# Optimization experiments

Measured on AMD Instinct MI355X. Metric: run time of the kernel, lower is better.

The kernel has to match this reference:

```python
import jax, jax.numpy as jnp
import numpy as np

OUT_H = 7
OUT_W = 7
C = 256
SPATIAL_SCALE = 0.0625
SAMPLING_RATIO = 2
GAMMA = 0.1
SIGMA = 0.5
FDIM = OUT_H * OUT_W * C  # 12544
DFC = 1024
B, H, W = 4, 100, 152
N_ROIS = 512
IMG_H, IMG_W = H / SPATIAL_SCALE, W / SPATIAL_SCALE


def _bilinear(feat, b, y, x):
    # feat: [B,H,W,C]; b int32 and y,x float coords, mutually broadcastable.
    Hf, Wf = feat.shape[1], feat.shape[2]
    valid = (y > -1.0) & (y < Hf) & (x > -1.0) & (x < Wf)
    yc = jnp.clip(y, 0.0, Hf - 1.0)
    xc = jnp.clip(x, 0.0, Wf - 1.0)
    y0 = jnp.clip(jnp.floor(yc).astype(jnp.int32), 0, Hf - 2)
    x0 = jnp.clip(jnp.floor(xc).astype(jnp.int32), 0, Wf - 2)
    ly = yc - y0.astype(yc.dtype)
    lx = xc - x0.astype(xc.dtype)
    hy, hx = 1.0 - ly, 1.0 - lx
    val = ((hy * hx)[..., None] * feat[b, y0, x0]
           + (hy * lx)[..., None] * feat[b, y0, x0 + 1]
           + (ly * hx)[..., None] * feat[b, y0 + 1, x0]
           + (ly * lx)[..., None] * feat[b, y0 + 1, x0 + 1])
    return jnp.where(valid[..., None], val, jnp.zeros((), val.dtype))


def deform_roi_pool(inp, rois, offset):
    # mmcv DeformRoIPool semantics; rois get no gradient (torch returns None).
    rois = jax.lax.stop_gradient(rois)
    feat = jnp.transpose(inp, (0, 2, 3, 1))  # [B,H,W,C]
    n = rois.shape[0]
    b = rois[:, 0].astype(jnp.int32)[:, None, None, None, None]
    x1 = rois[:, 1] * SPATIAL_SCALE - 0.5
    y1 = rois[:, 2] * SPATIAL_SCALE - 0.5
    x2 = rois[:, 3] * SPATIAL_SCALE - 0.5
    y2 = rois[:, 4] * SPATIAL_SCALE - 0.5
    rw, rh = x2 - x1, y2 - y1
    bw, bh = rw / OUT_W, rh / OUT_H
    start_w = jnp.broadcast_to(x1[:, None, None], (n, OUT_H, OUT_W))
    start_h = jnp.broadcast_to(y1[:, None, None], (n, OUT_H, OUT_W))
    if offset is not None:
        start_w = start_w + GAMMA * rw[:, None, None] * offset[:, 0]
        start_h = start_h + GAMMA * rh[:, None, None] * offset[:, 1]
    g = (jnp.arange(SAMPLING_RATIO, dtype=inp.dtype) + 0.5) / SAMPLING_RATIO
    ph = jnp.arange(OUT_H, dtype=inp.dtype)
    pw = jnp.arange(OUT_W, dtype=inp.dtype)
    # per-bin sample coords: ys,xs -> [n,oh,ow,g]
    ys = start_h[..., None] + (ph[None, :, None, None] + g) * bh[:, None, None, None]
    xs = start_w[..., None] + (pw[None, None, :, None] + g) * bw[:, None, None, None]
    yy = ys[..., :, None]  # [n,oh,ow,g,1]
    xx = xs[..., None, :]  # [n,oh,ow,1,g]
    val = _bilinear(feat, b, yy, xx)  # [n,oh,ow,g,g,C]
    out = val.mean(axis=(3, 4))  # count = g*g samples per bin
    return jnp.transpose(out, (0, 3, 1, 2))  # [n,C,oh,ow]


def _make_rois(key, n):
    k1, k2, k3, k4, k5 = jax.random.split(key, 5)
    bi = jax.random.randint(k1, (n,), 0, B).astype(jnp.float32)
    cx = jax.random.uniform(k2, (n,)) * IMG_W
    cy = jax.random.uniform(k3, (n,)) * IMG_H
    w = 32.0 + jax.random.uniform(k4, (n,)) * 300.0
    h = 32.0 + jax.random.uniform(k5, (n,)) * 300.0
    x1 = jnp.clip(cx - 0.5 * w, 0.0, IMG_W - 1.0)
    x2 = jnp.clip(cx + 0.5 * w, 0.0, IMG_W - 1.0)
    y1 = jnp.clip(cy - 0.5 * h, 0.0, IMG_H - 1.0)
    y2 = jnp.clip(cy + 0.5 * h, 0.0, IMG_H - 1.0)
    return jnp.stack([bi, x1, y1, x2, y2], axis=1)


def setup_inputs() -> dict:
    key = jax.random.key(0)
    ks = jax.random.split(key, 12)
    inp = jax.random.normal(ks[0], (B, C, H, W), dtype=jnp.float32)
    rois = _make_rois(ks[1], N_ROIS)
    s = 0.02
    return {
        'input': inp,
        'rois': rois,
        'rescale_w': s * jax.random.normal(ks[2], (OUT_H * OUT_W * 2, FDIM), jnp.float32),
        'rescale_b': s * jax.random.normal(ks[3], (OUT_H * OUT_W * 2,), jnp.float32),
        'off_w1': s * jax.random.normal(ks[4], (DFC, FDIM), jnp.float32),
        'off_b1': s * jax.random.normal(ks[5], (DFC,), jnp.float32),
        'off_w2': s * jax.random.normal(ks[6], (DFC, DFC), jnp.float32),
        'off_b2': s * jax.random.normal(ks[7], (DFC,), jnp.float32),
        'off_w3': s * jax.random.normal(ks[8], (OUT_H * OUT_W * 2, DFC), jnp.float32),
        'off_b3': s * jax.random.normal(ks[9], (OUT_H * OUT_W * 2,), jnp.float32),
    }


def reference(input, rois, rescale_w, rescale_b, off_w1, off_b1, off_w2, off_b2, off_w3, off_b3):
    x_cls = deform_roi_pool(input, rois, None)  # [N,C,7,7]
    n = rois.shape[0]
    flat = x_cls.reshape(n, -1)  # torch .view(N,-1) on NCHW layout
    rescale = 1.0 + SIGMA * jax.nn.sigmoid(flat @ rescale_w.T + rescale_b)
    # rescale_roi uses only columns 0..3 of the rescale head output
    cx = (rois[:, 1] + rois[:, 3]) * 0.5 + rescale[:, 0]
    cy = (rois[:, 2] + rois[:, 4]) * 0.5 + rescale[:, 1]
    nw = (rois[:, 3] - rois[:, 1]) * rescale[:, 2]
    nh = (rois[:, 4] - rois[:, 2]) * rescale[:, 3]
    new_rois = jnp.stack([rois[:, 0], cx - 0.5 * nw, cy - 0.5 * nh,
                          cx + 0.5 * nw, cy + 0.5 * nh], axis=-1)
    h1 = jax.nn.relu(flat @ off_w1.T + off_b1)
    h2 = jax.nn.relu(h1 @ off_w2.T + off_b2)
    off = (h2 @ off_w3.T + off_b3).reshape(n, 2, OUT_H, OUT_W)
    x_reg = deform_roi_pool(input, new_rois, off)
    return x_cls, x_reg
```

## Files before the change

### kernel.cpp

```cpp
#include <hip/hip_runtime.h>
#include <math.h>

#define NCH 256
#define HH 100
#define WW 152
#define BB 4
#define NROIS 512
#define FDIM 12544
#define DFC 1024
#define HW 15200

typedef unsigned short u16;
typedef float f32x2 __attribute__((ext_vector_type(2)));
typedef float f32x4 __attribute__((ext_vector_type(4)));
typedef short s16x8 __attribute__((ext_vector_type(8)));
typedef __bf16 bf16x8 __attribute__((ext_vector_type(8)));

__device__ __forceinline__ u16 f2bf(float f) {
  union { float f; unsigned u; } c; c.f = f;
  unsigned u = c.u;
  return (u16)((u + 0x7FFFu + ((u >> 16) & 1u)) >> 16);
}
__device__ __forceinline__ float bf2f(u16 h) {
  union { unsigned u; float f; } c; c.u = ((unsigned)h) << 16;
  return c.f;
}

template<int WITH_OFF>
__global__ __launch_bounds__(256) void pool_nchw(
    const float* __restrict__ feat, const float* __restrict__ rois,
    const float* __restrict__ offp, float* __restrict__ out) {
  const int n    = blockIdx.x;
  const int tid  = threadIdx.x;
  const int wave = tid >> 6;
  const int lane = tid & 63;
  float r[5];
  const float* rp = rois + n * 5;
  #pragma unroll
  for (int i = 0; i < 5; ++i) r[i] = rp[i];
  int b = (int)r[0];
  b = min(max(b, 0), BB - 1);
  const float x1 = r[1] * 0.0625f - 0.5f;
  const float y1 = r[2] * 0.0625f - 0.5f;
  const float x2 = r[3] * 0.0625f - 0.5f;
  const float y2 = r[4] * 0.0625f - 0.5f;
  const float rw = x2 - x1, rh = y2 - y1;
  const float bw = rw * (1.0f / 7.0f), bh = rh * (1.0f / 7.0f);
  const int bin = lane;
  const bool active = (bin < 49);
  const int ph = bin / 7;
  const int pw = bin - ph * 7;
  float sw = x1, sh = y1;
  if (WITH_OFF && active) {
    sw += 0.1f * rw * offp[n * 98 + bin];
    sh += 0.1f * rh * offp[n * 98 + 49 + bin];
  }
  int idx[4];
  float wt[4][4];
  bool val[4];
  #pragma unroll
  for (int s = 0; s < 4; ++s) {
    const int i = s >> 1, j = s & 1;
    const float y = sh + ((float)ph + 0.25f + 0.5f * (float)i) * bh;
    const float x = sw + ((float)pw + 0.25f + 0.5f * (float)j) * bw;
    val[s] = active && (y > -1.0f) && (y < (float)HH) && (x > -1.0f) && (x < (float)WW);
    float yc = fminf(fmaxf(y, 0.f), (float)(HH - 1));
    float xc = fminf(fmaxf(x, 0.f), (float)(WW - 1));
    int y0 = min(max((int)floorf(yc), 0), HH - 2);
    int x0 = min(max((int)floorf(xc), 0), WW - 2);
    const float ly = yc - (float)y0, lx = xc - (float)x0;
    const float hy = 1.f - ly, hx = 1.f - lx;
    idx[s] = y0 * WW + x0;
    wt[s][0] = hy * hx; wt[s][1] = hy * lx;
    wt[s][2] = ly * hx; wt[s][3] = ly * lx;
  }
  const float* fb = feat + (size_t)b * NCH * HW;
  float* op = out + (size_t)n * FDIM;
  for (int c = wave; c < NCH; c += 4) {
    const float* plane = fb + (size_t)c * HW;
    float acc = 0.f;
    #pragma unroll
    for (int s = 0; s < 4; ++s) {
      if (val[s]) {
        const float* p = plane + idx[s];
        acc += wt[s][0] * p[0] + wt[s][1] * p[1]
             + wt[s][2] * p[WW] + wt[s][3] * p[WW + 1];
      }
    }
    if (active) op[c * 49 + bin] = acc * 0.25f;
  }
}

__global__ __launch_bounds__(256) void nchw_to_nhwc(
    const float* __restrict__ in, float* __restrict__ outp) {
  __shared__ float tile[64][65];
  const int b  = blockIdx.z;
  const int c0 = blockIdx.y * 64;
  const int p0 = blockIdx.x * 64;
  const int tx = threadIdx.x & 63;
  const int ty = threadIdx.x >> 6;
  const float* ib = in + ((size_t)b * NCH + c0) * HW + p0;
  #pragma unroll
  for (int i = 0; i < 16; ++i) {
    const int r = ty + i * 4;
    tile[r][tx] = (p0 + tx < HW) ? ib[(size_t)r * HW + tx] : 0.f;
  }
  __syncthreads();
  float* ob = outp + ((size_t)b * HW + p0) * NCH + c0;
  #pragma unroll
  for (int i = 0; i < 16; ++i) {
    const int pr = ty + i * 4;
    if (p0 + pr < HW) ob[(size_t)pr * NCH + tx] = tile[tx][pr];
  }
}

template<int WITH_OFF, int SPLIT>
__global__ __launch_bounds__(256) void pool_nhwc_cg(
    const float* __restrict__ feat, const float* __restrict__ rois,
    const float* __restrict__ offp, float* __restrict__ out,
    u16* __restrict__ ahi, u16* __restrict__ alo) {
  __shared__ float obuf[64 * 49];
  const int n  = blockIdx.x;
  const int cg = blockIdx.y;
  const int w    = threadIdx.x >> 6;
  const int lane = threadIdx.x & 63;
  const int c = cg * 64 + lane;
  float r[5];
  const float* rp = rois + n * 5;
  #pragma unroll
  for (int i = 0; i < 5; ++i) r[i] = rp[i];
  int b = (int)r[0];
  b = min(max(b, 0), BB - 1);
  const float x1 = r[1] * 0.0625f - 0.5f;
  const float y1 = r[2] * 0.0625f - 0.5f;
  const float x2 = r[3] * 0.0625f - 0.5f;
  const float y2 = r[4] * 0.0625f - 0.5f;
  const float rw = x2 - x1, rh = y2 - y1;
  const float bw = rw * (1.0f / 7.0f), bh = rh * (1.0f / 7.0f);
  const float* fb = feat + (size_t)b * HW * NCH + c;
  for (int bin = w; bin < 49; bin += 4) {
    const int ph = bin / 7;
    const int pw = bin - ph * 7;
    float sw = x1, sh = y1;
    if (WITH_OFF) {
      sw += 0.1f * rw * offp[n * 98 + bin];
      sh += 0.1f * rh * offp[n * 98 + 49 + bin];
    }
    float acc = 0.f;
    #pragma unroll
    for (int s = 0; s < 4; ++s) {
      const int i = s >> 1, j = s & 1;
      const float y = sh + ((float)ph + 0.25f + 0.5f * (float)i) * bh;
      const float x = sw + ((float)pw + 0.25f + 0.5f * (float)j) * bw;
      const bool val = (y > -1.0f) && (y < (float)HH) && (x > -1.0f) && (x < (float)WW);
      float yc = fminf(fmaxf(y, 0.f), (float)(HH - 1));
      float xc = fminf(fmaxf(x, 0.f), (float)(WW - 1));
      int y0 = min(max((int)floorf(yc), 0), HH - 2);
      int x0 = min(max((int)floorf(xc), 0), WW - 2);
      const float ly = yc - (float)y0, lx = xc - (float)x0;
      const float hy = 1.f - ly, hx = 1.f - lx;
      if (val) {
        const float* p = fb + ((size_t)y0 * WW + x0) * NCH;
        acc += (hy * hx) * p[0] + (hy * lx) * p[NCH]
             + (ly * hx) * p[WW * NCH] + (ly * lx) * p[WW * NCH + NCH];
      }
    }
    obuf[lane * 49 + bin] = acc * 0.25f;
  }
  __syncthreads();
  const size_t base = (size_t)n * FDIM + (size_t)cg * (64 * 49);
  float* op = out + base;
  for (int i = threadIdx.x; i < 64 * 49; i += 256) {
    const float v = obuf[i];
    op[i] = v;
    if (SPLIT) {
      const u16 h = f2bf(v);
      ahi[base + i] = h;
      alo[base + i] = f2bf(v - bf2f(h));
    }
  }
}

__global__ __launch_bounds__(256) void rescale_rois_kernel(
    const float* __restrict__ flat, const float* __restrict__ w,
    const float* __restrict__ bsc, const float* __restrict__ rois,
    float* __restrict__ new_rois) {
  __shared__ float red[4];
  const int n = blockIdx.x;
  const int j = threadIdx.x >> 6;
  const int lane = threadIdx.x & 63;
  const float* a = flat + (size_t)n * FDIM;
  const float* wj = w + (size_t)j * FDIM;
  float acc = 0.f;
  for (int k = lane * 8; k + 8 <= FDIM; k += 64 * 8) {
    f32x4 a0 = *(const f32x4*)(a + k);
    f32x4 a1 = *(const f32x4*)(a + k + 4);
    f32x4 w0 = *(const f32x4*)(wj + k);
    f32x4 w1 = *(const f32x4*)(wj + k + 4);
    float s = 0.f;
    #pragma unroll
    for (int e = 0; e < 4; ++e) s += a0[e] * w0[e];
    #pragma unroll
    for (int e = 0; e < 4; ++e) s += a1[e] * w1[e];
    acc += s;
  }
  #pragma unroll
  for (int d = 32; d > 0; d >>= 1)
    acc += __shfl_down(acc, d, 64);
  if (lane == 0) red[j] = acc;
  __syncthreads();
  if (threadIdx.x == 0) {
    float rr[5];
    const float* rp = rois + n * 5;
    #pragma unroll
    for (int i = 0; i < 5; ++i) rr[i] = rp[i];
    float sc[4];
    #pragma unroll
    for (int jj = 0; jj < 4; ++jj) {
      const float z = red[jj] + bsc[jj];
      sc[jj] = 1.0f + 0.5f / (1.0f + expf(-z));
    }
    const float cx = (rr[1] + rr[3]) * 0.5f + sc[0];
    const float cy = (rr[2] + rr[4]) * 0.5f + sc[1];
    const float nw = (rr[3] - rr[1]) * sc[2];
    const float nh = (rr[4] - rr[2]) * sc[3];
    float* o = new_rois + n * 5;
    o[0] = rr[0];
    o[1] = cx - 0.5f * nw;
    o[2] = cy - 0.5f * nh;
    o[3] = cx + 0.5f * nw;
    o[4] = cy + 0.5f * nh;
  }
}

__global__ __launch_bounds__(512, 4) void gemm_mfma_sk(
    const float* __restrict__ A, const float* __restrict__ B,
    float* __restrict__ part, int M, int N, int Ns, int K, int kchunk) {
  __shared__ __align__(16) u16 Ah[64 * 32];
  __shared__ __align__(16) u16 Al[64 * 32];
  __shared__ __align__(16) u16 Bh[128 * 32];
  __shared__ __align__(16) u16 Bl[128 * 32];
  const int tid  = threadIdx.x;
  const int wave = tid >> 6;
  const int lane = tid & 63;
  const int q  = lane >> 4;
  const int rr = lane & 15;
  const int wr = wave >> 2;
  const int wc = wave & 3;
  const int m0 = blockIdx.y * 64;
  const int n0 = blockIdx.x * 128;
  const int s  = blockIdx.z;
  const int kb = s * kchunk, ke = kb + kchunk;

  const int srow  = tid >> 2;
  const int sslot = tid & 3;
  const int swz   = sslot ^ ((srow >> 1) & 3);
  const bool astage = tid < 256;
  u16* const a_sth = &Ah[srow * 32 + swz * 8];
  u16* const a_stl = &Al[srow * 32 + swz * 8];
  u16* const b_sth = &Bh[srow * 32 + swz * 8];
  u16* const b_stl = &Bl[srow * 32 + swz * 8];
  const float* Ap = A + (size_t)(m0 + (astage ? srow : 0)) * K + sslot * 8;
  const int  brow = n0 + srow;
  const bool bok  = brow < N;
  const float* Bp = B + (size_t)(bok ? brow : 0) * K + sslot * 8;

  const int rsw = q ^ ((rr >> 1) & 3);
  const u16* const a_rdh = &Ah[(wr * 32 + rr) * 32 + rsw * 8];
  const u16* const a_rdl = &Al[(wr * 32 + rr) * 32 + rsw * 8];
  const u16* const b_rdh = &Bh[(wc * 32 + rr) * 32 + rsw * 8];
  const u16* const b_rdl = &Bl[(wc * 32 + rr) * 32 + rsw * 8];

  f32x4 acc[2][2];
  #pragma unroll
  for (int mt = 0; mt < 2; ++mt)
    #pragma unroll
    for (int nt = 0; nt < 2; ++nt) acc[mt][nt] = (f32x4){0.f, 0.f, 0.f, 0.f};

  for (int k0 = kb; k0 < ke; k0 += 32) {
    f32x4 a0 = (f32x4){0.f, 0.f, 0.f, 0.f}, a1 = a0, b0 = a0, b1 = a0;
    if (astage) { a0 = *(const f32x4*)(Ap + k0); a1 = *(const f32x4*)(Ap + k0 + 4); }
    if (bok)    { b0 = *(const f32x4*)(Bp + k0); b1 = *(const f32x4*)(Bp + k0 + 4); }
    bf16x8 avh, avl, bvh, bvl;
    #pragma unroll
    for (int e = 0; e < 4; ++e) {
      const __bf16 h0 = (__bf16)a0[e], h1 = (__bf16)a1[e];
      avh[e] = h0; avh[e + 4] = h1;
      avl[e]     = (__bf16)(a0[e] - (float)h0);
      avl[e + 4] = (__bf16)(a1[e] - (float)h1);
      const __bf16 g0 = (__bf16)b0[e], g1 = (__bf16)b1[e];
      bvh[e] = g0; bvh[e + 4] = g1;
      bvl[e]     = (__bf16)(b0[e] - (float)g0);
      bvl[e + 4] = (__bf16)(b1[e] - (float)g1);
    }
    __syncthreads();
    if (astage) { *(bf16x8*)a_sth = avh; *(bf16x8*)a_stl = avl; }
    *(bf16x8*)b_sth = bvh;
    *(bf16x8*)b_stl = bvl;
    __syncthreads();
    bf16x8 ah[2], al[2], bh[2], bl[2];
    #pragma unroll
    for (int mt = 0; mt < 2; ++mt) {
      ah[mt] = *(const bf16x8*)(a_rdh + mt * 16 * 32);
      al[mt] = *(const bf16x8*)(a_rdl + mt * 16 * 32);
    }
    #pragma unroll
    for (int nt = 0; nt < 2; ++nt) {
      bh[nt] = *(const bf16x8*)(b_rdh + nt * 16 * 32);
      bl[nt] = *(const bf16x8*)(b_rdl + nt * 16 * 32);
    }
    #pragma unroll
    for (int mt = 0; mt < 2; ++mt)
      #pragma unroll
      for (int nt = 0; nt < 2; ++nt) {
        acc[mt][nt] = __builtin_amdgcn_mfma_f32_16x16x32_bf16(ah[mt], bh[nt], acc[mt][nt], 0, 0, 0);
        acc[mt][nt] = __builtin_amdgcn_mfma_f32_16x16x32_bf16(al[mt], bh[nt], acc[mt][nt], 0, 0, 0);
        acc[mt][nt] = __builtin_amdgcn_mfma_f32_16x16x32_bf16(ah[mt], bl[nt], acc[mt][nt], 0, 0, 0);
      }
  }

  float* pb = part + (size_t)s * M * Ns;
  #pragma unroll
  for (int mt = 0; mt < 2; ++mt)
    #pragma unroll
    for (int nt = 0; nt < 2; ++nt) {
      const int col = n0 + wc * 32 + nt * 16 + rr;
      #pragma unroll
      for (int i = 0; i < 4; ++i) {
        const int row = m0 + wr * 32 + mt * 16 + q * 4 + i;
        pb[(size_t)row * Ns + col] = acc[mt][nt][i];
      }
    }
}

__global__ __launch_bounds__(512) void gemm_mfma_ps_sk(
    const u16* __restrict__ Ahi, const u16* __restrict__ Alo,
    const float* __restrict__ B,
    float* __restrict__ part, int M, int N, int Ns, int K, int kchunk) {
  __shared__ __align__(16) u16 AhB[2][64 * 32];
  __shared__ __align__(16) u16 AlB[2][64 * 32];
  __shared__ __align__(16) u16 BhB[2][128 * 32];
  __shared__ __align__(16) u16 BlB[2][128 * 32];
  const int tid  = threadIdx.x;
  const int wave = tid >> 6;
  const int lane = tid & 63;
  const int q  = lane >> 4;
  const int rr = lane & 15;
  const int wr = wave >> 2;
  const int wc = wave & 3;
  const int m0 = blockIdx.y * 64;
  const int n0 = blockIdx.x * 128;
  const int s  = blockIdx.z;
  const int kb = s * kchunk, ke = kb + kchunk;

  const int srow  = tid >> 2;
  const int sslot = tid & 3;
  const int swz   = sslot ^ ((srow >> 1) & 3);
  const bool astage = tid < 256;
  const int ast = srow * 32 + swz * 8;
  const u16* Aph = Ahi + (size_t)(m0 + (astage ? srow : 0)) * K + sslot * 8;
  const u16* Apl = Alo + (size_t)(m0 + (astage ? srow : 0)) * K + sslot * 8;
  const int  brow = n0 + srow;
  const bool bok  = brow < N;
  const float* Bp = B + (size_t)(bok ? brow : 0) * K + sslot * 8;

  const int rsw = q ^ ((rr >> 1) & 3);
  const int ard = (wr * 32 + rr) * 32 + rsw * 8;
  const int brd = (wc * 32 + rr) * 32 + rsw * 8;

  f32x4 acc[2][2];
  #pragma unroll
  for (int mt = 0; mt < 2; ++mt)
    #pragma unroll
    for (int nt = 0; nt < 2; ++nt) acc[mt][nt] = (f32x4){0.f, 0.f, 0.f, 0.f};

  {
    s16x8 avh, avl;
    f32x4 b0 = (f32x4){0.f, 0.f, 0.f, 0.f}, b1 = b0;
    if (astage) { avh = *(const s16x8*)(Aph + kb); avl = *(const s16x8*)(Apl + kb); }
    if (bok)    { b0 = *(const f32x4*)(Bp + kb); b1 = *(const f32x4*)(Bp + kb + 4); }
    bf16x8 bvh, bvl;
    #pragma unroll
    for (int e = 0; e < 4; ++e) {
      const __bf16 g0 = (__bf16)b0[e], g1 = (__bf16)b1[e];
      bvh[e] = g0; bvh[e + 4] = g1;
      bvl[e]     = (__bf16)(b0[e] - (float)g0);
      bvl[e + 4] = (__bf16)(b1[e] - (float)g1);
    }
    if (astage) { *(s16x8*)&AhB[0][ast] = avh; *(s16x8*)&AlB[0][ast] = avl; }
    *(bf16x8*)&BhB[0][ast] = bvh;
    *(bf16x8*)&BlB[0][ast] = bvl;
  }
  __syncthreads();

  int cur = 0;
  for (int k0 = kb; k0 < ke; k0 += 32) {
    const bool nx = (k0 + 32 < ke);
    s16x8 navh, navl;
    f32x4 nb0 = (f32x4){0.f, 0.f, 0.f, 0.f}, nb1 = nb0;
    if (nx) {
      if (astage) {
        navh = *(const s16x8*)(Aph + k0 + 32);
        navl = *(const s16x8*)(Apl + k0 + 32);
      }
      if (bok) {
        nb0 = *(const f32x4*)(Bp + k0 + 32);
        nb1 = *(const f32x4*)(Bp + k0 + 36);
      }
    }
    bf16x8 ah[2], al[2], bh2[2], bl2[2];
    #pragma unroll
    for (int mt = 0; mt < 2; ++mt) {
      ah[mt] = *(const bf16x8*)&AhB[cur][ard + mt * 16 * 32];
      al[mt] = *(const bf16x8*)&AlB[cur][ard + mt * 16 * 32];
    }
    #pragma unroll
    for (int nt = 0; nt < 2; ++nt) {
      bh2[nt] = *(const bf16x8*)&BhB[cur][brd + nt * 16 * 32];
      bl2[nt] = *(const bf16x8*)&BlB[cur][brd + nt * 16 * 32];
    }
    #pragma unroll
    for (int mt = 0; mt < 2; ++mt)
      #pragma unroll
      for (int nt = 0; nt < 2; ++nt) {
        acc[mt][nt] = __builtin_amdgcn_mfma_f32_16x16x32_bf16(ah[mt], bh2[nt], acc[mt][nt], 0, 0, 0);
        acc[mt][nt] = __builtin_amdgcn_mfma_f32_16x16x32_bf16(al[mt], bh2[nt], acc[mt][nt], 0, 0, 0);
        acc[mt][nt] = __builtin_amdgcn_mfma_f32_16x16x32_bf16(ah[mt], bl2[nt], acc[mt][nt], 0, 0, 0);
      }
    if (nx) {
      bf16x8 nbvh, nbvl;
      #pragma unroll
      for (int e = 0; e < 4; ++e) {
        const __bf16 g0 = (__bf16)nb0[e], g1 = (__bf16)nb1[e];
        nbvh[e] = g0; nbvh[e + 4] = g1;
        nbvl[e]     = (__bf16)(nb0[e] - (float)g0);
        nbvl[e + 4] = (__bf16)(nb1[e] - (float)g1);
      }
      if (astage) { *(s16x8*)&AhB[cur ^ 1][ast] = navh; *(s16x8*)&AlB[cur ^ 1][ast] = navl; }
      *(bf16x8*)&BhB[cur ^ 1][ast] = nbvh;
      *(bf16x8*)&BlB[cur ^ 1][ast] = nbvl;
    }
    __syncthreads();
    cur ^= 1;
  }

  float* pb = part + (size_t)s * M * Ns;
  #pragma unroll
  for (int mt = 0; mt < 2; ++mt)
    #pragma unroll
    for (int nt = 0; nt < 2; ++nt) {
      const int col = n0 + wc * 32 + nt * 16 + rr;
      #pragma unroll
      for (int i = 0; i < 4; ++i) {
        const int row = m0 + wr * 32 + mt * 16 + q * 4 + i;
        pb[(size_t)row * Ns + col] = acc[mt][nt][i];
      }
    }
}

template<int RELU>
__global__ __launch_bounds__(256) void reduce_sk(
    const float* __restrict__ part, const float* __restrict__ bias,
    float* __restrict__ out, int M, int N, int Ns, int S) {
  const int idx = blockIdx.x * 256 + threadIdx.x;
  if (idx >= M * Ns) return;
  const int m = idx / Ns, n = idx - m * Ns;
  if (n >= N) return;
  float v = bias[n];
  for (int s = 0; s < S; ++s) v += part[(size_t)s * M * Ns + idx];
  if (RELU) v = fmaxf(v, 0.f);
  out[(size_t)m * N + n] = v;
}

__global__ __launch_bounds__(256) void reduce_sk_split(
    const float* __restrict__ part, const float* __restrict__ bias,
    u16* __restrict__ oh, u16* __restrict__ ol, int M, int N, int S) {
  const int idx = blockIdx.x * 256 + threadIdx.x;
  if (idx >= M * N) return;
  const int n = idx % N;
  float v = bias[n];
  for (int s = 0; s < S; ++s) v += part[(size_t)s * M * N + idx];
  v = fmaxf(v, 0.f);
  const u16 h = f2bf(v);
  oh[idx] = h;
  ol[idx] = f2bf(v - bf2f(h));
}

extern "C" void kernel_launch(void* const* d_in, const int* in_sizes, int n_in,
                              void* d_out, int out_size, void* d_ws, size_t ws_size,
                              hipStream_t stream) {
  const float* input  = (const float*)d_in[0];
  const float* rois   = (const float*)d_in[1];
  const float* resc_w = (const float*)d_in[2];
  const float* resc_b = (const float*)d_in[3];
  const float* w1     = (const float*)d_in[4];
  const float* b1     = (const float*)d_in[5];
  const float* w2     = (const float*)d_in[6];
  const float* b2     = (const float*)d_in[7];
  const float* w3     = (const float*)d_in[8];
  const float* b3     = (const float*)d_in[9];
  float* out = (float*)d_out;

  char* ws = (char*)d_ws;
  const size_t feat_t_bytes = (size_t)BB * HW * NCH * sizeof(float);

  float* part    = (float*)ws;
  u16*   h1h     = (u16*)(ws + (16u << 20));
  u16*   h1l     = (u16*)(ws + (17u << 20));
  u16*   h2h     = (u16*)(ws + (18u << 20));
  u16*   h2l     = (u16*)(ws + (19u << 20));
  float* offbuf2 = (float*)(ws + (20u << 20));
  float* nrois2  = (float*)(ws + (20u << 20) + 512 * 1024);
  u16*   Ahi     = (u16*)(ws + (21u << 20));
  u16*   Alo     = (u16*)(ws + (34u << 20));
  float* feat_t2 = (float*)(ws + (47u << 20));
  const bool big2 = ws_size >= ((size_t)(47u << 20) + feat_t_bytes);

  float* h1     = (float*)(ws + (16u << 20));
  float* h2     = (float*)(ws + (18u << 20));
  float* offbuf = (float*)(ws + (22u << 20));
  float* nrois  = (float*)(ws + (22u << 20) + 256 * 1024);
  float* feat_t = (float*)(ws + ((size_t)24 << 20));
  const bool big = ws_size >= (((size_t)24 << 20) + feat_t_bytes);

  float* x_cls = out;
  float* x_reg = out + (size_t)NROIS * FDIM;

  if (big2) {
    nchw_to_nhwc<<<dim3(238, 4, 4), 256, 0, stream>>>(input, feat_t2);
    pool_nhwc_cg<0, 1><<<dim3(NROIS, 4), 256, 0, stream>>>(feat_t2, rois, nullptr, x_cls, Ahi, Alo);
    rescale_rois_kernel<<<NROIS, 256, 0, stream>>>(x_cls, resc_w, resc_b, rois, nrois2);

    gemm_mfma_ps_sk<<<dim3(8, 8, 8), 512, 0, stream>>>(Ahi, Alo, w1, part, NROIS, DFC, DFC, FDIM, FDIM / 8);
    reduce_sk_split<<<(NROIS * DFC + 255) / 256, 256, 0, stream>>>(part, b1, h1h, h1l, NROIS, DFC, 8);
    gemm_mfma_ps_sk<<<dim3(8, 8, 8), 512, 0, stream>>>(h1h, h1l, w2, part, NROIS, DFC, DFC, DFC, DFC / 8);
    reduce_sk_split<<<(NROIS * DFC + 255) / 256, 256, 0, stream>>>(part, b2, h2h, h2l, NROIS, DFC, 8);
    gemm_mfma_ps_sk<<<dim3(1, 8, 8), 512, 0, stream>>>(h2h, h2l, w3, part, NROIS, 98, 128, DFC, DFC / 8);
    reduce_sk<0><<<(NROIS * 128 + 255) / 256, 256, 0, stream>>>(part, b3, offbuf2, NROIS, 98, 128, 8);

    pool_nhwc_cg<1, 0><<<dim3(NROIS, 4), 256, 0, stream>>>(feat_t2, nrois2, offbuf2, x_reg, nullptr, nullptr);
  } else if (big) {
    nchw_to_nhwc<<<dim3(238, 4, 4), 256, 0, stream>>>(input, feat_t);
    pool_nhwc_cg<0, 0><<<dim3(NROIS, 4), 256, 0, stream>>>(feat_t, rois, nullptr, x_cls, nullptr, nullptr);
    rescale_rois_kernel<<<NROIS, 256, 0, stream>>>(x_cls, resc_w, resc_b, rois, nrois);

    gemm_mfma_sk<<<dim3(8, 8, 8), 512, 0, stream>>>(x_cls, w1, part, NROIS, DFC, DFC, FDIM, FDIM / 8);
    reduce_sk<1><<<(NROIS * DFC + 255) / 256, 256, 0, stream>>>(part, b1, h1, NROIS, DFC, DFC, 8);
    gemm_mfma_sk<<<dim3(8, 8, 8), 512, 0, stream>>>(h1, w2, part, NROIS, DFC, DFC, DFC, DFC / 8);
    reduce_sk<1><<<(NROIS * DFC + 255) / 256, 256, 0, stream>>>(part, b2, h2, NROIS, DFC, DFC, 8);
    gemm_mfma_sk<<<dim3(1, 8, 8), 512, 0, stream>>>(h2, w3, part, NROIS, 98, 128, DFC, DFC / 8);
    reduce_sk<0><<<(NROIS * 128 + 255) / 256, 256, 0, stream>>>(part, b3, offbuf, NROIS, 98, 128, 8);

    pool_nhwc_cg<1, 0><<<dim3(NROIS, 4), 256, 0, stream>>>(feat_t, nrois, offbuf, x_reg, nullptr, nullptr);
  } else {
    pool_nchw<0><<<NROIS, 256, 0, stream>>>(input, rois, nullptr, x_cls);
    rescale_rois_kernel<<<NROIS, 256, 0, stream>>>(x_cls, resc_w, resc_b, rois, nrois);
    gemm_mfma_sk<<<dim3(8, 8, 8), 512, 0, stream>>>(x_cls, w1, part, NROIS, DFC, DFC, FDIM, FDIM / 8);
    reduce_sk<1><<<(NROIS * DFC + 255) / 256, 256, 0, stream>>>(part, b1, h1, NROIS, DFC, DFC, 8);
    gemm_mfma_sk<<<dim3(8, 8, 8), 512, 0, stream>>>(h1, w2, part, NROIS, DFC, DFC, DFC, DFC / 8);
    reduce_sk<1><<<(NROIS * DFC + 255) / 256, 256, 0, stream>>>(part, b2, h2, NROIS, DFC, DFC, 8);
    gemm_mfma_sk<<<dim3(1, 8, 8), 512, 0, stream>>>(h2, w3, part, NROIS, 98, 128, DFC, DFC / 8);
    reduce_sk<0><<<(NROIS * 128 + 255) / 256, 256, 0, stream>>>(part, b3, offbuf, NROIS, 98, 128, 8);
    pool_nchw<1><<<NROIS, 256, 0, stream>>>(input, nrois, offbuf, x_reg);
  }
}
```

Baseline: 359.0 us.

## Single-buffer split-precision GEMM, raise occupancy, and deepen split-K for first layer

Replaces the register-prefetched double-buffered LDS pipeline in the split-bf16 GEMM with a single-buffered loop that loads, stores and syncs twice per K step. It adds a launch-bounds occupancy hint of 4 blocks per CU. When the workspace is large enough, the first FC layer's split-K factor goes from 8 to 14 to launch more blocks, using a larger partial-sum buffer. The aim is more resident waves to hide latency, at the cost of losing explicit prefetch overlap and an extra barrier per iteration.

```diff
diff --git a/kernel.cpp b/kernel.cpp
--- a/kernel.cpp
+++ b/kernel.cpp
@@ -11,7 +11,6 @@
 #define HW 15200
 
 typedef unsigned short u16;
-typedef float f32x2 __attribute__((ext_vector_type(2)));
 typedef float f32x4 __attribute__((ext_vector_type(4)));
 typedef short s16x8 __attribute__((ext_vector_type(8)));
 typedef __bf16 bf16x8 __attribute__((ext_vector_type(8)));
@@ -333,14 +332,14 @@
     }
 }
 
-__global__ __launch_bounds__(512) void gemm_mfma_ps_sk(
+__global__ __launch_bounds__(512, 4) void gemm_ps(
     const u16* __restrict__ Ahi, const u16* __restrict__ Alo,
     const float* __restrict__ B,
     float* __restrict__ part, int M, int N, int Ns, int K, int kchunk) {
-  __shared__ __align__(16) u16 AhB[2][64 * 32];
-  __shared__ __align__(16) u16 AlB[2][64 * 32];
-  __shared__ __align__(16) u16 BhB[2][128 * 32];
-  __shared__ __align__(16) u16 BlB[2][128 * 32];
+  __shared__ __align__(16) u16 Ah[64 * 32];
+  __shared__ __align__(16) u16 Al[64 * 32];
+  __shared__ __align__(16) u16 Bh[128 * 32];
+  __shared__ __align__(16) u16 Bl[128 * 32];
   const int tid  = threadIdx.x;
   const int wave = tid >> 6;
   const int lane = tid & 63;
@@ -357,7 +356,10 @@
   const int sslot = tid & 3;
   const int swz   = sslot ^ ((srow >> 1) & 3);
   const bool astage = tid < 256;
-  const int ast = srow * 32 + swz * 8;
+  u16* const a_sth = &Ah[srow * 32 + swz * 8];
+  u16* const a_stl = &Al[srow * 32 + swz * 8];
+  u16* const b_sth = &Bh[srow * 32 + swz * 8];
+  u16* const b_stl = &Bl[srow * 32 + swz * 8];
   const u16* Aph = Ahi + (size_t)(m0 + (astage ? srow : 0)) * K + sslot * 8;
   const u16* Apl = Alo + (size_t)(m0 + (astage ? srow : 0)) * K + sslot * 8;
   const int  brow = n0 + srow;
@@ -365,8 +367,10 @@
   const float* Bp = B + (size_t)(bok ? brow : 0) * K + sslot * 8;
 
   const int rsw = q ^ ((rr >> 1) & 3);
-  const int ard = (wr * 32 + rr) * 32 + rsw * 8;
-  const int brd = (wc * 32 + rr) * 32 + rsw * 8;
+  const u16* const a_rdh = &Ah[(wr * 32 + rr) * 32 + rsw * 8];
+  const u16* const a_rdl = &Al[(wr * 32 + rr) * 32 + rsw * 8];
+  const u16* const b_rdh = &Bh[(wc * 32 + rr) * 32 + rsw * 8];
+  const u16* const b_rdl = &Bl[(wc * 32 + rr) * 32 + rsw * 8];
 
   f32x4 acc[2][2];
   #pragma unroll
@@ -374,11 +378,11 @@
     #pragma unroll
     for (int nt = 0; nt < 2; ++nt) acc[mt][nt] = (f32x4){0.f, 0.f, 0.f, 0.f};
 
-  {
+  for (int k0 = kb; k0 < ke; k0 += 32) {
     s16x8 avh, avl;
     f32x4 b0 = (f32x4){0.f, 0.f, 0.f, 0.f}, b1 = b0;
-    if (astage) { avh = *(const s16x8*)(Aph + kb); avl = *(const s16x8*)(Apl + kb); }
-    if (bok)    { b0 = *(const f32x4*)(Bp + kb); b1 = *(const f32x4*)(Bp + kb + 4); }
+    if (astage) { avh = *(const s16x8*)(Aph + k0); avl = *(const s16x8*)(Apl + k0); }
+    if (bok)    { b0 = *(const f32x4*)(Bp + k0); b1 = *(const f32x4*)(Bp + k0 + 4); }
     bf16x8 bvh, bvl;
     #pragma unroll
     for (int e = 0; e < 4; ++e) {
@@ -387,61 +391,30 @@
       bvl[e]     = (__bf16)(b0[e] - (float)g0);
       bvl[e + 4] = (__bf16)(b1[e] - (float)g1);
     }
-    if (astage) { *(s16x8*)&AhB[0][ast] = avh; *(s16x8*)&AlB[0][ast] = avl; }
-    *(bf16x8*)&BhB[0][ast] = bvh;
-    *(bf16x8*)&BlB[0][ast] = bvl;
-  }
-  __syncthreads();
-
-  int cur = 0;
-  for (int k0 = kb; k0 < ke; k0 += 32) {
-    const bool nx = (k0 + 32 < ke);
-    s16x8 navh, navl;
-    f32x4 nb0 = (f32x4){0.f, 0.f, 0.f, 0.f}, nb1 = nb0;
-    if (nx) {
-      if (astage) {
-        navh = *(const s16x8*)(Aph + k0 + 32);
-        navl = *(const s16x8*)(Apl + k0 + 32);
-      }
-      if (bok) {
-        nb0 = *(const f32x4*)(Bp + k0 + 32);
-        nb1 = *(const f32x4*)(Bp + k0 + 36);
-      }
-    }
-    bf16x8 ah[2], al[2], bh2[2], bl2[2];
+    __syncthreads();
+    if (astage) { *(s16x8*)a_sth = avh; *(s16x8*)a_stl = avl; }
+    *(bf16x8*)b_sth = bvh;
+    *(bf16x8*)b_stl = bvl;
+    __syncthreads();
+    bf16x8 ah[2], al[2], bh[2], bl[2];
     #pragma unroll
     for (int mt = 0; mt < 2; ++mt) {
-      ah[mt] = *(const bf16x8*)&AhB[cur][ard + mt * 16 * 32];
-      al[mt] = *(const bf16x8*)&AlB[cur][ard + mt * 16 * 32];
+      ah[mt] = *(const bf16x8*)(a_rdh + mt * 16 * 32);
+      al[mt] = *(const bf16x8*)(a_rdl + mt * 16 * 32);
     }
     #pragma unroll
     for (int nt = 0; nt < 2; ++nt) {
-      bh2[nt] = *(const bf16x8*)&BhB[cur][brd + nt * 16 * 32];
-      bl2[nt] = *(const bf16x8*)&BlB[cur][brd + nt * 16 * 32];
+      bh[nt] = *(const bf16x8*)(b_rdh + nt * 16 * 32);
+      bl[nt] = *(const bf16x8*)(b_rdl + nt * 16 * 32);
     }
     #pragma unroll
     for (int mt = 0; mt < 2; ++mt)
       #pragma unroll
       for (int nt = 0; nt < 2; ++nt) {
-        acc[mt][nt] = __builtin_amdgcn_mfma_f32_16x16x32_bf16(ah[mt], bh2[nt], acc[mt][nt], 0, 0, 0);
-        acc[mt][nt] = __builtin_amdgcn_mfma_f32_16x16x32_bf16(al[mt], bh2[nt], acc[mt][nt], 0, 0, 0);
-        acc[mt][nt] = __builtin_amdgcn_mfma_f32_16x16x32_bf16(ah[mt], bl2[nt], acc[mt][nt], 0, 0, 0);
+        acc[mt][nt] = __builtin_amdgcn_mfma_f32_16x16x32_bf16(ah[mt], bh[nt], acc[mt][nt], 0, 0, 0);
+        acc[mt][nt] = __builtin_amdgcn_mfma_f32_16x16x32_bf16(al[mt], bh[nt], acc[mt][nt], 0, 0, 0);
+        acc[mt][nt] = __builtin_amdgcn_mfma_f32_16x16x32_bf16(ah[mt], bl[nt], acc[mt][nt], 0, 0, 0);
       }
-    if (nx) {
-      bf16x8 nbvh, nbvl;
-      #pragma unroll
-      for (int e = 0; e < 4; ++e) {
-        const __bf16 g0 = (__bf16)nb0[e], g1 = (__bf16)nb1[e];
-        nbvh[e] = g0; nbvh[e + 4] = g1;
-        nbvl[e]     = (__bf16)(nb0[e] - (float)g0);
-        nbvl[e + 4] = (__bf16)(nb1[e] - (float)g1);
-      }
-      if (astage) { *(s16x8*)&AhB[cur ^ 1][ast] = navh; *(s16x8*)&AlB[cur ^ 1][ast] = navl; }
-      *(bf16x8*)&BhB[cur ^ 1][ast] = nbvh;
-      *(bf16x8*)&BlB[cur ^ 1][ast] = nbvl;
-    }
-    __syncthreads();
-    cur ^= 1;
   }
 
   float* pb = part + (size_t)s * M * Ns;
@@ -504,42 +477,64 @@
   char* ws = (char*)d_ws;
   const size_t feat_t_bytes = (size_t)BB * HW * NCH * sizeof(float);
 
-  float* part    = (float*)ws;
-  u16*   h1h     = (u16*)(ws + (16u << 20));
-  u16*   h1l     = (u16*)(ws + (17u << 20));
-  u16*   h2h     = (u16*)(ws + (18u << 20));
-  u16*   h2l     = (u16*)(ws + (19u << 20));
-  float* offbuf2 = (float*)(ws + (20u << 20));
-  float* nrois2  = (float*)(ws + (20u << 20) + 512 * 1024);
-  u16*   Ahi     = (u16*)(ws + (21u << 20));
-  u16*   Alo     = (u16*)(ws + (34u << 20));
-  float* feat_t2 = (float*)(ws + (47u << 20));
-  const bool big2 = ws_size >= ((size_t)(47u << 20) + feat_t_bytes);
-
-  float* h1     = (float*)(ws + (16u << 20));
-  float* h2     = (float*)(ws + (18u << 20));
-  float* offbuf = (float*)(ws + (22u << 20));
-  float* nrois  = (float*)(ws + (22u << 20) + 256 * 1024);
-  float* feat_t = (float*)(ws + ((size_t)24 << 20));
-  const bool big = ws_size >= (((size_t)24 << 20) + feat_t_bytes);
-
   float* x_cls = out;
   float* x_reg = out + (size_t)NROIS * FDIM;
 
-  if (big2) {
+  const bool big3 = ws_size >= (((size_t)59 << 20) + feat_t_bytes);
+  const bool big2 = ws_size >= (((size_t)47 << 20) + feat_t_bytes);
+  const bool big = ws_size >= (((size_t)24 << 20) + feat_t_bytes);
+
+  if (big3 || big2) {
+    float* part;
+    u16 *h1h, *h1l, *h2h, *h2l, *Ahi, *Alo;
+    float *offbuf2, *nrois2, *feat_t2;
+    int S1;
+    if (big3) {
+      part    = (float*)ws;
+      h1h     = (u16*)(ws + ((size_t)28 << 20));
+      h1l     = (u16*)(ws + ((size_t)29 << 20));
+      h2h     = (u16*)(ws + ((size_t)30 << 20));
+      h2l     = (u16*)(ws + ((size_t)31 << 20));
+      offbuf2 = (float*)(ws + ((size_t)32 << 20));
+      nrois2  = (float*)(ws + ((size_t)32 << 20) + 512 * 1024);
+      Ahi     = (u16*)(ws + ((size_t)33 << 20));
+      Alo     = (u16*)(ws + ((size_t)46 << 20));
+      feat_t2 = (float*)(ws + ((size_t)59 << 20));
+      S1 = 14;
+    } else {
+      part    = (float*)ws;
+      h1h     = (u16*)(ws + ((size_t)16 << 20));
+      h1l     = (u16*)(ws + ((size_t)17 << 20));
+      h2h     = (u16*)(ws + ((size_t)18 << 20));
+      h2l     = (u16*)(ws + ((size_t)19 << 20));
+      offbuf2 = (float*)(ws + ((size_t)20 << 20));
+      nrois2  = (float*)(ws + ((size_t)20 << 20) + 512 * 1024);
+      Ahi     = (u16*)(ws + ((size_t)21 << 20));
+      Alo     = (u16*)(ws + ((size_t)34 << 20));
+      feat_t2 = (float*)(ws + ((size_t)47 << 20));
+      S1 = 8;
+    }
+
     nchw_to_nhwc<<<dim3(238, 4, 4), 256, 0, stream>>>(input, feat_t2);
     pool_nhwc_cg<0, 1><<<dim3(NROIS, 4), 256, 0, stream>>>(feat_t2, rois, nullptr, x_cls, Ahi, Alo);
     rescale_rois_kernel<<<NROIS, 256, 0, stream>>>(x_cls, resc_w, resc_b, rois, nrois2);
 
-    gemm_mfma_ps_sk<<<dim3(8, 8, 8), 512, 0, stream>>>(Ahi, Alo, w1, part, NROIS, DFC, DFC, FDIM, FDIM / 8);
-    reduce_sk_split<<<(NROIS * DFC + 255) / 256, 256, 0, stream>>>(part, b1, h1h, h1l, NROIS, DFC, 8);
-    gemm_mfma_ps_sk<<<dim3(8, 8, 8), 512, 0, stream>>>(h1h, h1l, w2, part, NROIS, DFC, DFC, DFC, DFC / 8);
+    gemm_ps<<<dim3(8, 8, S1), 512, 0, stream>>>(Ahi, Alo, w1, part, NROIS, DFC, DFC, FDIM, FDIM / S1);
+    reduce_sk_split<<<(NROIS * DFC + 255) / 256, 256, 0, stream>>>(part, b1, h1h, h1l, NROIS, DFC, S1);
+    gemm_ps<<<dim3(8, 8, 8), 512, 0, stream>>>(h1h, h1l, w2, part, NROIS, DFC, DFC, DFC, DFC / 8);
     reduce_sk_split<<<(NROIS * DFC + 255) / 256, 256, 0, stream>>>(part, b2, h2h, h2l, NROIS, DFC, 8);
-    gemm_mfma_ps_sk<<<dim3(1, 8, 8), 512, 0, stream>>>(h2h, h2l, w3, part, NROIS, 98, 128, DFC, DFC / 8);
+    gemm_ps<<<dim3(1, 8, 8), 512, 0, stream>>>(h2h, h2l, w3, part, NROIS, 98, 128, DFC, DFC / 8);
     reduce_sk<0><<<(NROIS * 128 + 255) / 256, 256, 0, stream>>>(part, b3, offbuf2, NROIS, 98, 128, 8);
 
     pool_nhwc_cg<1, 0><<<dim3(NROIS, 4), 256, 0, stream>>>(feat_t2, nrois2, offbuf2, x_reg, nullptr, nullptr);
   } else if (big) {
+    float* part   = (float*)ws;
+    float* h1     = (float*)(ws + ((size_t)16 << 20));
+    float* h2     = (float*)(ws + ((size_t)18 << 20));
+    float* offbuf = (float*)(ws + ((size_t)22 << 20));
+    float* nrois  = (float*)(ws + ((size_t)22 << 20) + 256 * 1024);
+    float* feat_t = (float*)(ws + ((size_t)24 << 20));
+
     nchw_to_nhwc<<<dim3(238, 4, 4), 256, 0, stream>>>(input, feat_t);
     pool_nhwc_cg<0, 0><<<dim3(NROIS, 4), 256, 0, stream>>>(feat_t, rois, nullptr, x_cls, nullptr, nullptr);
     rescale_rois_kernel<<<NROIS, 256, 0, stream>>>(x_cls, resc_w, resc_b, rois, nrois);
@@ -553,6 +548,12 @@
 
     pool_nhwc_cg<1, 0><<<dim3(NROIS, 4), 256, 0, stream>>>(feat_t, nrois, offbuf, x_reg, nullptr, nullptr);
   } else {
+    float* part   = (float*)ws;
+    float* h1     = (float*)(ws + ((size_t)16 << 20));
+    float* h2     = (float*)(ws + ((size_t)18 << 20));
+    float* offbuf = (float*)(ws + ((size_t)22 << 20));
+    float* nrois  = (float*)(ws + ((size_t)22 << 20) + 256 * 1024);
+
     pool_nchw<0><<<NROIS, 256, 0, stream>>>(input, rois, nullptr, x_cls);
     rescale_rois_kernel<<<NROIS, 256, 0, stream>>>(x_cls, resc_w, resc_b, rois, nrois);
     gemm_mfma_sk<<<dim3(8, 8, 8), 512, 0, stream>>>(x_cls, w1, part, NROIS, DFC, DFC, FDIM, FDIM / 8);
```

Result: no change. 362.0 us (+0.8%).
